# Optimization experiments

Measured on AMD Instinct MI355X. Metric: run time of the kernel, lower is better.

The kernel has to match this reference:

```python
import jax, jax.numpy as jnp
import numpy as np

N, E = 50000, 800000          # nodes, edges (avg degree 16)
D_IN, D_H = 128, 128          # input_size, hidden_size


def setup_inputs() -> dict:
    key = jax.random.key(0)
    ks = jax.random.split(key, 10)
    s = 0.05  # param init scale
    return {
        "x": jax.random.normal(ks[0], (N, D_IN), jnp.float32),
        "edge_index": jax.random.randint(ks[1], (2, E), 0, N, jnp.int32),
        "h_prev": jax.random.normal(ks[2], (N, D_H), jnp.float32),
        # reset gate params: xr (Linear with bias), hr (no bias)
        "W_xr": jax.random.normal(ks[3], (D_IN, D_H), jnp.float32) * s,
        "b_xr": jnp.zeros((D_H,), jnp.float32),
        "W_hr": jax.random.normal(ks[4], (D_H, D_H), jnp.float32) * s,
        # update gate params
        "W_xz": jax.random.normal(ks[5], (D_IN, D_H), jnp.float32) * s,
        "b_xz": jnp.zeros((D_H,), jnp.float32),
        "W_hz": jax.random.normal(ks[6], (D_H, D_H), jnp.float32) * s,
        # SAGEConv params: lin_l on mean-aggregated neighbors (bias), lin_r on root (no bias)
        "W_l": jax.random.normal(ks[7], (D_IN + D_H, D_H), jnp.float32) * s,
        "b_l": jnp.zeros((D_H,), jnp.float32),
        "W_r": jax.random.normal(ks[8], (D_IN + D_H, D_H), jnp.float32) * s,
    }


def reference(x, edge_index, h_prev, W_xr, b_xr, W_hr, W_xz, b_xz, W_hz, W_l, b_l, W_r):
    # GRU-style gates
    r = jax.nn.sigmoid(x @ W_xr + b_xr + h_prev @ W_hr)   # [N, D_H]
    z = jax.nn.sigmoid(x @ W_xz + b_xz + h_prev @ W_hz)   # [N, D_H]

    # candidate via single-layer GraphSAGE (SAGEConv, mean aggregation)
    xc = jnp.concatenate([x, r * h_prev], axis=-1)        # [N, D_IN+D_H]
    src, dst = edge_index[0], edge_index[1]
    agg = jax.ops.segment_sum(xc[src], dst, num_segments=N)              # [N, D_IN+D_H]
    cnt = jax.ops.segment_sum(jnp.ones((E,), xc.dtype), dst, num_segments=N)
    mean_nbr = agg / jnp.maximum(cnt, 1.0)[:, None]
    # PyG BasicGNN applies no activation after the last (only) layer, so no tanh here.
    n = mean_nbr @ W_l + b_l + xc @ W_r                   # [N, D_H]

    return (1.0 - z) * n + z * h_prev
```

## Files before the change

### kernel.cpp

```cpp
#include <hip/hip_runtime.h>
#include <hip/hip_bf16.h>

typedef __attribute__((ext_vector_type(8))) short bf16x8;
typedef __attribute__((ext_vector_type(4))) short s16x4;
typedef __attribute__((ext_vector_type(4))) float f32x4;
typedef __attribute__((ext_vector_type(4))) int i32x4;
typedef unsigned short u16;
typedef unsigned int u32;

#define D 128
#define DC 256
#define TILES 8
#define SWZ(row, dim) (((row) << 7) + ((dim) ^ (((row) & 15) << 3)))

__device__ __forceinline__ float bf2f(u16 b) {
    u32 u = ((u32)b) << 16;
    return __uint_as_float(u);
}
__device__ __forceinline__ u16 f2bf(float f) {
    u32 u = __float_as_uint(f);
    u32 r = (u + 0x7fffu + ((u >> 16) & 1u)) >> 16;
    return (u16)r;
}
__device__ __forceinline__ float sigmoidf_(float x) {
    float e = __builtin_amdgcn_exp2f(-1.4426950408889634f * x);
    return __builtin_amdgcn_rcpf(1.0f + e);
}
__device__ __forceinline__ bf16x8 cvt8(const float* __restrict__ p) {
    f32x4 lo = *(const f32x4*)p;
    f32x4 hi = *(const f32x4*)(p + 4);
    union { bf16x8 v; u16 s[8]; } u;
#pragma unroll
    for (int i = 0; i < 4; i++) {
        u.s[i]     = f2bf(lo[i]);
        u.s[i + 4] = f2bf(hi[i]);
    }
    return u.v;
}

__global__ __launch_bounds__(256) void prep_kernel(
    const float* __restrict__ Wxr, const float* __restrict__ Whr,
    const float* __restrict__ Wxz, const float* __restrict__ Whz,
    const float* __restrict__ Wl,  const float* __restrict__ Wr,
    u16* __restrict__ WxrT, u16* __restrict__ WhrT,
    u16* __restrict__ WxzT, u16* __restrict__ WhzT,
    u16* __restrict__ WlT,  u16* __restrict__ WrT,
    const int* __restrict__ ei, int* __restrict__ deg,
    int E)
{
    int bid = blockIdx.x;
    int tid = threadIdx.x;
    if (bid < 64) {
        int m = bid >> 4;
        int idx = (bid & 15) * 1024 + tid * 4;
        const float* W = (m == 0) ? Wxr : (m == 1) ? Whr : (m == 2) ? Wxz : Whz;
        u16* Wt        = (m == 0) ? WxrT : (m == 1) ? WhrT : (m == 2) ? WxzT : WhzT;
        f32x4 v = *(const f32x4*)(W + idx);
        int k = idx >> 7, n = idx & 127;
#pragma unroll
        for (int j = 0; j < 4; j++) Wt[(n + j) * D + k] = f2bf(v[j]);
    } else if (bid < 128) {
        int m = (bid - 64) >> 5;
        int idx = ((bid - 64) & 31) * 1024 + tid * 4;
        const float* W = (m == 0) ? Wl : Wr;
        u16* Wt        = (m == 0) ? WlT : WrT;
        f32x4 v = *(const f32x4*)(W + idx);
        int k = idx >> 7, n = idx & 127;
#pragma unroll
        for (int j = 0; j < 4; j++) Wt[(n + j) * DC + k] = f2bf(v[j]);
    } else {
        long long e = ((long long)(bid - 128) * 256 + tid) * 4;
        if (e + 3 < E) {
            i32x4 d4 = *(const i32x4*)(ei + (size_t)E + e);
#pragma unroll
            for (int j = 0; j < 4; j++) atomicAdd(&deg[d4[j]], 1);
        } else {
            for (int j = 0; j < 4 && e + j < E; j++)
                atomicAdd(&deg[ei[(size_t)E + e + j]], 1);
        }
    }
}

__global__ __launch_bounds__(256) void scan1_kernel(
    const int* __restrict__ deg, int* __restrict__ rstart,
    int* __restrict__ bsum, int N)
{
    __shared__ int tmp[256];
    int t = threadIdx.x;
    int g = blockIdx.x * 256 + t;
    int v = (g < N) ? deg[g] : 0;
    tmp[t] = v;
    __syncthreads();
#pragma unroll
    for (int s = 1; s < 256; s <<= 1) {
        int add = (t >= s) ? tmp[t - s] : 0;
        __syncthreads();
        tmp[t] += add;
        __syncthreads();
    }
    if (g < N) rstart[g] = tmp[t] - v;
    if (t == 255) bsum[blockIdx.x] = tmp[255];
}

__global__ __launch_bounds__(256) void scan23_kernel(
    int* __restrict__ rstart, const int* __restrict__ bsum, int N, int nbn)
{
    __shared__ int tmp[256];
    int t = threadIdx.x;
    int v = (t < nbn) ? bsum[t] : 0;
    tmp[t] = v;
    __syncthreads();
#pragma unroll
    for (int s = 1; s < 256; s <<= 1) {
        int add = (t >= s) ? tmp[t - s] : 0;
        __syncthreads();
        tmp[t] += add;
        __syncthreads();
    }
    int b = blockIdx.x;
    int excl = tmp[b] - ((b < nbn) ? bsum[b] : 0);
    int g = b * 256 + t;
    if (g < N) rstart[g] += excl;
}

__global__ __launch_bounds__(256) void fill_kernel(
    const int* __restrict__ ei, int* __restrict__ rstart,
    int* __restrict__ col, int E)
{
    long long e = ((long long)blockIdx.x * 256 + threadIdx.x) * 4;
    if (e + 3 < E) {
        i32x4 s4 = *(const i32x4*)(ei + e);
        i32x4 d4 = *(const i32x4*)(ei + (size_t)E + e);
#pragma unroll
        for (int j = 0; j < 4; j++) {
            int pos = atomicAdd(&rstart[d4[j]], 1);
            col[pos] = s4[j];
        }
    } else {
        for (long long q = e; q < E; q++) {
            int pos = atomicAdd(&rstart[ei[(size_t)E + q]], 1);
            col[pos] = ei[q];
        }
    }
}

__global__ __launch_bounds__(512, 4) void fused_kernel(
    const float* __restrict__ x, const float* __restrict__ h,
    const u16* __restrict__ WxrT, const u16* __restrict__ WhrT,
    const u16* __restrict__ WxzT, const u16* __restrict__ WhzT,
    const u16* __restrict__ WlT,  const u16* __restrict__ WrT,
    const float* __restrict__ bxr, const float* __restrict__ bxz,
    u16* __restrict__ zo, u16* __restrict__ yo, u16* __restrict__ wo, int N)
{
    __shared__ u16 xT[TILES][16 * 128];
    __shared__ u16 hT[TILES][16 * 128];
    const int wave = threadIdx.x >> 6;
    const int lane = threadIdx.x & 63;
    const int quad = lane >> 4;
    const int l15  = lane & 15;
    const int node0 = blockIdx.x * (TILES * 16);
    if (node0 >= N) return;

    {
        int tb = node0 + wave * 16;
        u16* Lx = xT[wave];
        u16* Lh = hT[wave];
#pragma unroll
        for (int it = 0; it < 4; it++) {
            int idx = it * 64 + lane;
            int row = idx >> 4, seg = idx & 15;
            int node = tb + row; if (node >= N) node = N - 1;
            *(bf16x8*)&Lx[SWZ(row, seg * 8)] = cvt8(x + (size_t)node * D + seg * 8);
            *(bf16x8*)&Lh[SWZ(row, seg * 8)] = cvt8(h + (size_t)node * D + seg * 8);
        }
    }
    __syncthreads();

    const int dim = wave * 16 + l15;
    u32 rhp0[TILES], rhp1[TILES];

    {
        const u16* wrx = WxrT + (size_t)dim * D + quad * 8;
        const u16* wrh = WhrT + (size_t)dim * D + quad * 8;
        const u16* wzx = WxzT + (size_t)dim * D + quad * 8;
        const u16* wzh = WhzT + (size_t)dim * D + quad * 8;
        bf16x8 b0[4], b1[4], b2[4], b3[4];
#pragma unroll
        for (int c = 0; c < 4; c++) {
            b0[c] = *(const bf16x8*)(wrx + c * 32);
            b1[c] = *(const bf16x8*)(wrh + c * 32);
            b2[c] = *(const bf16x8*)(wzx + c * 32);
            b3[c] = *(const bf16x8*)(wzh + c * 32);
        }
        float br = bxr[dim];
        float bz = bxz[dim];
#pragma unroll
        for (int t = 0; t < TILES; t++) {
            const u16* Lx = xT[t];
            const u16* Lh = hT[t];
            int tb = node0 + t * 16;
            bf16x8 ax[4], ah[4];
#pragma unroll
            for (int c = 0; c < 4; c++) {
                ax[c] = *(const bf16x8*)&Lx[SWZ(l15, c * 32 + quad * 8)];
                ah[c] = *(const bf16x8*)&Lh[SWZ(l15, c * 32 + quad * 8)];
            }
            f32x4 ar = {0.f,0.f,0.f,0.f};
            f32x4 az = {0.f,0.f,0.f,0.f};
#pragma unroll
            for (int c = 0; c < 4; c++) {
                ar = __builtin_amdgcn_mfma_f32_16x16x32_bf16(ax[c], b0[c], ar, 0, 0, 0);
                ar = __builtin_amdgcn_mfma_f32_16x16x32_bf16(ah[c], b1[c], ar, 0, 0, 0);
                az = __builtin_amdgcn_mfma_f32_16x16x32_bf16(ax[c], b2[c], az, 0, 0, 0);
                az = __builtin_amdgcn_mfma_f32_16x16x32_bf16(ah[c], b3[c], az, 0, 0, 0);
            }
            u32 p0 = 0, p1 = 0;
#pragma unroll
            for (int reg = 0; reg < 4; reg++) {
                int row = quad * 4 + reg;
                int node = tb + row;
                float hv = bf2f(Lh[SWZ(row, dim)]);
                float r  = sigmoidf_(ar[reg] + br);
                float zz = sigmoidf_(az[reg] + bz);
                u32 rh = f2bf(r * hv);
                if (reg == 0) p0 = rh;
                else if (reg == 1) p0 |= rh << 16;
                else if (reg == 2) p1 = rh;
                else p1 |= rh << 16;
                if (node < N) zo[(size_t)node * D + dim] = f2bf(zz);
            }
            rhp0[t] = p0;
            rhp1[t] = p1;
        }
    }
    __syncthreads();

#pragma unroll
    for (int t = 0; t < TILES; t++) {
        u16* Lh = hT[t];
        Lh[SWZ(quad * 4 + 0, dim)] = (u16)(rhp0[t]);
        Lh[SWZ(quad * 4 + 1, dim)] = (u16)(rhp0[t] >> 16);
        Lh[SWZ(quad * 4 + 2, dim)] = (u16)(rhp1[t]);
        Lh[SWZ(quad * 4 + 3, dim)] = (u16)(rhp1[t] >> 16);
    }
    __syncthreads();

    {
        const u16* pl = WlT + (size_t)dim * DC + quad * 8;
        const u16* pr = WrT + (size_t)dim * DC + quad * 8;
        bf16x8 l0[4], l1[4], r0[4], r1[4];
#pragma unroll
        for (int c = 0; c < 4; c++) {
            l0[c] = *(const bf16x8*)(pl + c * 32);
            l1[c] = *(const bf16x8*)(pl + 128 + c * 32);
            r0[c] = *(const bf16x8*)(pr + c * 32);
            r1[c] = *(const bf16x8*)(pr + 128 + c * 32);
        }
#pragma unroll
        for (int t = 0; t < TILES; t++) {
            const u16* Lx  = xT[t];
            const u16* Lrh = hT[t];
            int tb = node0 + t * 16;
            bf16x8 ax[4], arh[4];
#pragma unroll
            for (int c = 0; c < 4; c++) {
                ax[c]  = *(const bf16x8*)&Lx[SWZ(l15, c * 32 + quad * 8)];
                arh[c] = *(const bf16x8*)&Lrh[SWZ(l15, c * 32 + quad * 8)];
            }
            f32x4 ay = {0.f,0.f,0.f,0.f};
            f32x4 aw = {0.f,0.f,0.f,0.f};
#pragma unroll
            for (int c = 0; c < 4; c++) {
                ay = __builtin_amdgcn_mfma_f32_16x16x32_bf16(ax[c],  l0[c], ay, 0, 0, 0);
                ay = __builtin_amdgcn_mfma_f32_16x16x32_bf16(arh[c], l1[c], ay, 0, 0, 0);
                aw = __builtin_amdgcn_mfma_f32_16x16x32_bf16(ax[c],  r0[c], aw, 0, 0, 0);
                aw = __builtin_amdgcn_mfma_f32_16x16x32_bf16(arh[c], r1[c], aw, 0, 0, 0);
            }
#pragma unroll
            for (int reg = 0; reg < 4; reg++) {
                int row = quad * 4 + reg;
                int node = tb + row;
                if (node < N) {
                    yo[(size_t)node * D + dim] = f2bf(ay[reg]);
                    wo[(size_t)node * D + dim] = f2bf(aw[reg]);
                }
            }
        }
    }
}

__global__ __launch_bounds__(256) void pull_kernel(
    const int* __restrict__ rend, const int* __restrict__ deg,
    const int* __restrict__ col, const u16* __restrict__ y,
    const u16* __restrict__ z, const u16* __restrict__ w,
    const float* __restrict__ h, const float* __restrict__ bl,
    float* __restrict__ out, int N)
{
    const int wave = threadIdx.x >> 6;
    const int lane = threadIdx.x & 63;
    const int node = blockIdx.x * 4 + wave;
    if (node >= N) return;

    const int d    = deg[node];
    const int base = rend[node] - d;
    const int g    = lane >> 4;
    const int l15  = lane & 15;

    const int dcap = (d < 64) ? d : 64;
    int cols = 0;
    if (lane < dcap) cols = col[base + lane];

    float a[8] = {0.f,0.f,0.f,0.f,0.f,0.f,0.f,0.f};
    for (int i = 0; i < dcap; i += 8) {
        int e0 = i + g, e1 = i + 4 + g;
        int s0 = __shfl(cols, e0 & 63, 64);
        int s1 = __shfl(cols, e1 & 63, 64);
        bool v0 = e0 < dcap, v1 = e1 < dcap;
        bf16x8 A = {}, B = {};
        if (v0) A = *(const bf16x8*)(y + (size_t)s0 * D + l15 * 8);
        if (v1) B = *(const bf16x8*)(y + (size_t)s1 * D + l15 * 8);
        if (v0) {
#pragma unroll
            for (int j = 0; j < 8; j++) a[j] += bf2f((u16)A[j]);
        }
        if (v1) {
#pragma unroll
            for (int j = 0; j < 8; j++) a[j] += bf2f((u16)B[j]);
        }
    }
    for (int i = 64; i < d; i += 4) {
        int e = i + g;
        if (e < d) {
            int s = col[base + e];
            bf16x8 v = *(const bf16x8*)(y + (size_t)s * D + l15 * 8);
#pragma unroll
            for (int j = 0; j < 8; j++) a[j] += bf2f((u16)v[j]);
        }
    }
#pragma unroll
    for (int j = 0; j < 8; j++) {
        a[j] += __shfl_xor(a[j], 16, 64);
        a[j] += __shfl_xor(a[j], 32, 64);
    }
    if (lane < 16) {
        float inv = 1.0f / (float)(d > 0 ? d : 1);
        size_t o16 = (size_t)node * D + l15 * 8;
        bf16x8 zv = *(const bf16x8*)(z + o16);
        bf16x8 wv = *(const bf16x8*)(w + o16);
        f32x4 h0 = *(const f32x4*)(h + o16);
        f32x4 h1 = *(const f32x4*)(h + o16 + 4);
        f32x4 b0 = *(const f32x4*)(bl + l15 * 8);
        f32x4 b1 = *(const f32x4*)(bl + l15 * 8 + 4);
        f32x4 o0, o1;
#pragma unroll
        for (int j = 0; j < 4; j++) {
            float zz = bf2f((u16)zv[j]);
            float nv = a[j] * inv + b0[j] + bf2f((u16)wv[j]);
            o0[j] = (1.0f - zz) * nv + zz * h0[j];
        }
#pragma unroll
        for (int j = 0; j < 4; j++) {
            float zz = bf2f((u16)zv[j + 4]);
            float nv = a[j + 4] * inv + b1[j] + bf2f((u16)wv[j + 4]);
            o1[j] = (1.0f - zz) * nv + zz * h1[j];
        }
        *(f32x4*)(out + o16)     = o0;
        *(f32x4*)(out + o16 + 4) = o1;
    }
}

extern "C" void kernel_launch(void* const* d_in, const int* in_sizes, int n_in,
                              void* d_out, int out_size, void* d_ws, size_t ws_size,
                              hipStream_t stream)
{
    const float* x   = (const float*)d_in[0];
    const int*   ei  = (const int*)d_in[1];
    const float* h   = (const float*)d_in[2];
    const float* Wxr = (const float*)d_in[3];
    const float* bxr = (const float*)d_in[4];
    const float* Whr = (const float*)d_in[5];
    const float* Wxz = (const float*)d_in[6];
    const float* bxz = (const float*)d_in[7];
    const float* Whz = (const float*)d_in[8];
    const float* Wl  = (const float*)d_in[9];
    const float* bl  = (const float*)d_in[10];
    const float* Wr  = (const float*)d_in[11];
    float* out = (float*)d_out;

    const int N = in_sizes[0] / D;
    const int E = in_sizes[1] / 2;
    if (N <= 0 || E <= 0) return;

    const int nbn = (N + 255) / 256;
    if (nbn > 256) return;

    char* ws = (char*)d_ws;
    size_t off = 0;
    auto alloc = [&](size_t bytes) -> void* {
        void* p = ws + off;
        off += (bytes + 255) & ~(size_t)255;
        return p;
    };
    u16*   z     = (u16*)  alloc((size_t)N * D * 2);
    u16*   y     = (u16*)  alloc((size_t)N * D * 2);
    u16*   w     = (u16*)  alloc((size_t)N * D * 2);
    int*   deg   = (int*)  alloc((size_t)N * 4);
    int*   rstart= (int*)  alloc((size_t)N * 4);
    int*   bsum  = (int*)  alloc((size_t)256 * 4);
    int*   col   = (int*)  alloc((size_t)E * 4);
    u16*   WxrT  = (u16*)  alloc((size_t)D * D * 2);
    u16*   WhrT  = (u16*)  alloc((size_t)D * D * 2);
    u16*   WxzT  = (u16*)  alloc((size_t)D * D * 2);
    u16*   WhzT  = (u16*)  alloc((size_t)D * D * 2);
    u16*   WlT   = (u16*)  alloc((size_t)DC * D * 2);
    u16*   WrT   = (u16*)  alloc((size_t)DC * D * 2);
    (void)n_in; (void)out_size;
    if (off > ws_size) return;

    hipMemsetAsync(deg, 0, (size_t)N * 4, stream);

    const int nbh4 = (E + 1023) / 1024;
    prep_kernel<<<128 + nbh4, 256, 0, stream>>>(
        Wxr, Whr, Wxz, Whz, Wl, Wr,
        WxrT, WhrT, WxzT, WhzT, WlT, WrT,
        ei, deg, E);

    scan1_kernel<<<nbn, 256, 0, stream>>>(deg, rstart, bsum, N);
    scan23_kernel<<<nbn, 256, 0, stream>>>(rstart, bsum, N, nbn);
    fill_kernel<<<nbh4, 256, 0, stream>>>(ei, rstart, col, E);

    fused_kernel<<<(N + TILES * 16 - 1) / (TILES * 16), 512, 0, stream>>>(
        x, h, WxrT, WhrT, WxzT, WhzT, WlT, WrT, bxr, bxz, z, y, w, N);

    pull_kernel<<<(N + 3) / 4, 256, 0, stream>>>(
        rstart, deg, col, y, z, w, h, bl, out, N);
}
```

Baseline: 285.5 us.

## Partition CSR fill by destination range across blocks to localize atomics

The CSR fill kernel now launches 8 partitions per edge slice. Each block scans its slice of edges but only handles edges whose destination falls in its node range. Consecutive block IDs map to different partitions, so atomics and column writes from concurrently running blocks likely land in different regions of rstart and col, which may improve L2 locality. In exchange, each edge is read 8 times and the launch shape changes.

```diff
diff --git a/kernel.cpp b/kernel.cpp
--- a/kernel.cpp
+++ b/kernel.cpp
@@ -11,6 +11,7 @@
 #define D 128
 #define DC 256
 #define TILES 8
+#define NPART 8
 #define SWZ(row, dim) (((row) << 7) + ((dim) ^ (((row) & 15) << 3)))
 
 __device__ __forceinline__ float bf2f(u16 b) {
@@ -125,21 +126,33 @@
 
 __global__ __launch_bounds__(256) void fill_kernel(
     const int* __restrict__ ei, int* __restrict__ rstart,
-    int* __restrict__ col, int E)
-{
-    long long e = ((long long)blockIdx.x * 256 + threadIdx.x) * 4;
-    if (e + 3 < E) {
-        i32x4 s4 = *(const i32x4*)(ei + e);
-        i32x4 d4 = *(const i32x4*)(ei + (size_t)E + e);
-#pragma unroll
-        for (int j = 0; j < 4; j++) {
-            int pos = atomicAdd(&rstart[d4[j]], 1);
-            col[pos] = s4[j];
-        }
-    } else {
-        for (long long q = e; q < E; q++) {
-            int pos = atomicAdd(&rstart[ei[(size_t)E + q]], 1);
-            col[pos] = ei[q];
+    int* __restrict__ col, int E, int SL, int PSTEP)
+{
+    const int part = blockIdx.x & (NPART - 1);
+    const int sidx = blockIdx.x >> 3;
+    const int lo = part * PSTEP, hi = lo + PSTEP;
+    long long base = (long long)sidx * SL;
+    long long end  = base + SL; if (end > E) end = E;
+    for (long long e = base + threadIdx.x * 4; e < end; e += 1024) {
+        if (e + 4 <= end) {
+            i32x4 s4 = *(const i32x4*)(ei + e);
+            i32x4 d4 = *(const i32x4*)(ei + (size_t)E + e);
+#pragma unroll
+            for (int j = 0; j < 4; j++) {
+                int dd = d4[j];
+                if (dd >= lo && dd < hi) {
+                    int pos = atomicAdd(&rstart[dd], 1);
+                    col[pos] = s4[j];
+                }
+            }
+        } else {
+            for (long long q = e; q < end; q++) {
+                int dd = ei[(size_t)E + q];
+                if (dd >= lo && dd < hi) {
+                    int pos = atomicAdd(&rstart[dd], 1);
+                    col[pos] = ei[q];
+                }
+            }
         }
     }
 }
@@ -427,7 +440,11 @@
 
     scan1_kernel<<<nbn, 256, 0, stream>>>(deg, rstart, bsum, N);
     scan23_kernel<<<nbn, 256, 0, stream>>>(rstart, bsum, N, nbn);
-    fill_kernel<<<nbh4, 256, 0, stream>>>(ei, rstart, col, E);
+
+    const int nsl   = 98;
+    const int SL    = (((E + nsl - 1) / nsl) + 3) & ~3;
+    const int PSTEP = (N + NPART - 1) / NPART;
+    fill_kernel<<<NPART * nsl, 256, 0, stream>>>(ei, rstart, col, E, SL, PSTEP);
 
     fused_kernel<<<(N + TILES * 16 - 1) / (TILES * 16), 512, 0, stream>>>(
         x, h, WxrT, WhrT, WxzT, WhzT, WlT, WrT, bxr, bxz, z, y, w, N);
```

Result: faster. 274.0 us (-4.0%).
